# Optimization experiments

Hardware: AMD Instinct MI355X
Metric: run time of the kernel (lower is better)

Reference implementation:

```python
import jax, jax.numpy as jnp
import numpy as np

IMG = 224          # image_size
FMAP = (56, 56)    # feature_map_dims (AdaptiveAvgPool2d((56,56)))
K_REWEIGHT = 3     # self.n_reweight
BLUR_RADIUS = 4    # KNNGaussianBlur(4): kernel 9, sigma 4


def _cdist(a, b):
    # Euclidean pairwise distance, [Na, D] x [Nb, D] -> [Na, Nb]
    a2 = jnp.sum(a * a, axis=1, keepdims=True)            # [Na,1]
    b2 = jnp.sum(b * b, axis=1, keepdims=True).T          # [1,Nb]
    d2 = a2 + b2 - 2.0 * (a @ b.T)
    return jnp.sqrt(jnp.maximum(d2, 0.0))


def _gaussian_blur(x):
    # x: [1,1,H,W]; torchvision GaussianBlur(kernel=9, sigma=4), reflect pad
    r, sigma = BLUR_RADIUS, float(BLUR_RADIUS)
    t = jnp.arange(2 * r + 1, dtype=x.dtype) - r
    g = jnp.exp(-(t * t) / (2.0 * sigma * sigma))
    g = g / jnp.sum(g)
    k2d = jnp.outer(g, g)[None, None]                     # [1,1,9,9]
    xp = jnp.pad(x, ((0, 0), (0, 0), (r, r), (r, r)), mode='reflect')
    return jax.lax.conv_general_dilated(
        xp, k2d, window_strides=(1, 1), padding='VALID',
        dimension_numbers=('NCHW', 'OIHW', 'NCHW'))


def setup_inputs() -> dict:
    key = jax.random.key(0)
    k1, k2 = jax.random.split(key)
    patch = jax.random.normal(k1, (FMAP[0] * FMAP[1], 768), dtype=jnp.float32)
    patch_lib = jax.random.normal(k2, (16384, 768), dtype=jnp.float32)
    mean = jnp.zeros((), dtype=jnp.float32)
    std = jnp.ones((), dtype=jnp.float32)
    return {"patch": patch, "patch_lib": patch_lib, "mean": mean, "std": std}


def reference(patch, patch_lib, mean, std):
    # normalization (method_name != 'Point_MAE' branch)
    p = (patch - mean) / std                               # [N, D]

    dist = _cdist(p, patch_lib)                            # [N, Nlib]
    min_val = jnp.min(dist, axis=1)                        # [N]
    min_idx = jnp.argmin(dist, axis=1)                     # [N]
    s_idx = jnp.argmax(min_val)
    s_star = jnp.max(min_val)

    m_test = p[s_idx]                                      # [D]
    m_star = patch_lib[min_idx[s_idx]]                     # [D]

    # distances of m_star to whole bank, k smallest
    w_dist = jnp.sqrt(jnp.maximum(
        jnp.sum((patch_lib - m_star) ** 2, axis=1), 0.0))  # [Nlib]
    _, nn_idx = jax.lax.top_k(-w_dist, K_REWEIGHT)         # smallest k
    m_star_knn = jnp.linalg.norm(
        m_test[None, :] - patch_lib[nn_idx[1:]], axis=1)   # [k-1]

    D_sqrt = jnp.sqrt(jnp.asarray(patch.shape[1], dtype=p.dtype))
    w = 1.0 - jnp.exp(s_star / D_sqrt) / jnp.sum(jnp.exp(m_star_knn / D_sqrt))
    s = w * s_star

    s_map = min_val.reshape(1, 1, *FMAP)
    s_map = jax.image.resize(s_map, (1, 1, IMG, IMG), method='bilinear')
    s_map = _gaussian_blur(s_map)
    return s, s_map
```

## Files before the change

kernel.cpp:

```cpp
#include <hip/hip_runtime.h>
#include <hip/hip_bf16.h>
#include <stdint.h>

#define N_PATCH 3136
#define N_PATCH_PAD 3328
#define N_LIB   16384
#define DIM     768
#define IMGSZ   224
#define FM      56

#define TILE 256
#define BK 32
#define KT 24
#define MT 13
#define NTILES 64

#define TAILB 64
#define D2_MARGIN 8.0f

typedef __bf16 bf16_t;
typedef __bf16 bf16x8 __attribute__((ext_vector_type(8)));
typedef __bf16 bf16x4_v __attribute__((ext_vector_type(4)));
typedef float  f32x4  __attribute__((ext_vector_type(4)));

#define FLT_MAX_ 3.402823466e+38f

struct Scal {
  unsigned long long approx_max_pack;
  unsigned long long cand_pack[64];
  int cand[64];
  int cand_count;
  int bar[4];
};

__device__ __forceinline__ float wave_reduce_sum(float v) {
#pragma unroll
  for (int s = 32; s > 0; s >>= 1) v += __shfl_xor(v, s, 64);
  return v;
}

__device__ __forceinline__ float wave_reduce_min(float v) {
#pragma unroll
  for (int s = 32; s > 0; s >>= 1) v = fminf(v, __shfl_xor(v, s, 64));
  return v;
}

__device__ __forceinline__ unsigned long long shfl_xor_u64(unsigned long long v, int mask) {
  unsigned lo = (unsigned)v, hi = (unsigned)(v >> 32);
  lo = __shfl_xor(lo, mask, 64);
  hi = __shfl_xor(hi, mask, 64);
  return ((unsigned long long)hi << 32) | lo;
}

__device__ __forceinline__ void async16(const bf16_t* g, bf16_t* l) {
  __builtin_amdgcn_global_load_lds(
      (const __attribute__((address_space(1))) unsigned int*)g,
      (__attribute__((address_space(3))) unsigned int*)l, 16, 0, 0);
}

__device__ __forceinline__ void grid_bar(int* ctr, int nb) {
  __syncthreads();
  if (threadIdx.x == 0) {
    __threadfence();
    atomicAdd(ctr, 1);
    while (atomicAdd(ctr, 0) < nb) __builtin_amdgcn_s_sleep(8);
    __threadfence();
  }
  __syncthreads();
}

__device__ __forceinline__ float bf16u_to_f(unsigned short u) {
  return __uint_as_float(((unsigned)u) << 16);
}

__global__ void prep_kernel(const float* __restrict__ patch, const float* __restrict__ lib,
                            const float* __restrict__ meanp, const float* __restrict__ stdp,
                            bf16_t* __restrict__ pb, bf16_t* __restrict__ lb,
                            float* __restrict__ a2, float* __restrict__ b2, Scal* sc) {
  int t = threadIdx.x;
  int lane = t & 63;
  if (blockIdx.x == 0) {
    if (t < 64) sc->cand_pack[t] = ~0ULL;
    if (t == 64) { sc->approx_max_pack = 0ULL; sc->cand_count = 0; }
    if (t >= 65 && t < 69) sc->bar[t - 65] = 0;
  }
  if (blockIdx.x < N_PATCH / 4) {
    int row = blockIdx.x * 4 + (t >> 6);
    float mu = meanp[0], sd = stdp[0];
    float acc = 0.f;
#pragma unroll
    for (int k = 0; k < 3; k++) {
      float4 v = ((const float4*)(patch + (size_t)row * DIM))[lane + 64 * k];
      v.x = (v.x - mu) / sd; v.y = (v.y - mu) / sd;
      v.z = (v.z - mu) / sd; v.w = (v.w - mu) / sd;
      bf16x4_v o = {(__bf16)v.x, (__bf16)v.y, (__bf16)v.z, (__bf16)v.w};
      *(bf16x4_v*)(pb + (size_t)row * DIM + (lane + 64 * k) * 4) = o;
      acc += v.x*v.x + v.y*v.y + v.z*v.z + v.w*v.w;
    }
    acc = wave_reduce_sum(acc);
    if (lane == 0) a2[row] = acc;
  } else {
    int row = (blockIdx.x - N_PATCH / 4) * 4 + (t >> 6);
    float acc = 0.f;
#pragma unroll
    for (int k = 0; k < 3; k++) {
      float4 v = ((const float4*)(lib + (size_t)row * DIM))[lane + 64 * k];
      bf16x4_v o = {(__bf16)v.x, (__bf16)v.y, (__bf16)v.z, (__bf16)v.w};
      *(bf16x4_v*)(lb + (size_t)row * DIM + (lane + 64 * k) * 4) = o;
      acc += v.x*v.x + v.y*v.y + v.z*v.z + v.w*v.w;
    }
    acc = wave_reduce_sum(acc);
    if (lane == 0) b2[row] = acc;
  }
}

__global__ __launch_bounds__(512, 2)
void gemm_min_kernel(const bf16_t* __restrict__ pb, const bf16_t* __restrict__ lb,
                     const float* __restrict__ a2, const float* __restrict__ b2,
                     float* __restrict__ part) {
  __shared__ __align__(16) bf16_t As[4][TILE * BK];
  __shared__ __align__(16) bf16_t Bs[4][TILE * BK];

  const int t = threadIdx.x;
  const int wave = t >> 6;
  const int lane = t & 63;
  const int l15 = lane & 15;
  const int quad = lane >> 4;
  const int wm = (wave >> 2) * 128;
  const int wn = (wave & 3) * 64;

  const int lid = blockIdx.x;
  const int xcd = lid & 7;
  const int slot = lid >> 3;
  const int ntile = xcd + 8 * (slot / MT);
  const int mtile = slot % MT;
  const int m0 = mtile * TILE;
  const int n0 = ntile * TILE;

  int rA0, kA0, rA1, kA1;
  {
    int c = t, L = c >> 3, s = c & 7, g = s ^ (L & 7);
    rA0 = 2 * L + (g >> 2); kA0 = g & 3;
    c = t + 512; L = c >> 3; s = c & 7; g = s ^ (L & 7);
    rA1 = 2 * L + (g >> 2); kA1 = g & 3;
  }
  int raA0 = m0 + rA0;        if (raA0 > N_PATCH - 1) raA0 = N_PATCH - 1;
  int raA1 = m0 + rA1;        if (raA1 > N_PATCH - 1) raA1 = N_PATCH - 1;
  const bf16_t* gA0 = pb + (size_t)raA0 * DIM + kA0 * 8;
  const bf16_t* gA1 = pb + (size_t)raA1 * DIM + kA1 * 8;
  const bf16_t* gB0 = lb + (size_t)(n0 + rA0) * DIM + kA0 * 8;
  const bf16_t* gB1 = lb + (size_t)(n0 + rA1) * DIM + kA1 * 8;

  auto stage = [&](int kt, int s) {
    const size_t ko = (size_t)kt * BK;
    async16(gA0 + ko, &As[s][0] + (size_t)t * 8);
    async16(gA1 + ko, &As[s][0] + 4096 + (size_t)t * 8);
    async16(gB0 + ko, &Bs[s][0] + (size_t)t * 8);
    async16(gB1 + ko, &Bs[s][0] + 4096 + (size_t)t * 8);
  };

  const int off_lane = (l15 >> 1) * 128 + (((((l15 & 1) << 2) | quad) ^ (l15 >> 1)) << 4);

  f32x4 acc[8][4];
#pragma unroll
  for (int mi = 0; mi < 8; mi++)
#pragma unroll
    for (int ni = 0; ni < 4; ni++) { f32x4 z = {0.f,0.f,0.f,0.f}; acc[mi][ni] = z; }

  stage(0, 0); stage(1, 1); stage(2, 2);

  auto compute = [&](int s) {
    const char* Ab = (const char*)(&As[s][0]);
    const char* Bb = (const char*)(&Bs[s][0]);
    bf16x8 afr[8], bfr[4];
#pragma unroll
    for (int ni = 0; ni < 4; ni++)
      bfr[ni] = *(const bf16x8*)(Bb + (wn + ni * 16) * 64 + off_lane);
#pragma unroll
    for (int mi = 0; mi < 8; mi++)
      afr[mi] = *(const bf16x8*)(Ab + (wm + mi * 16) * 64 + off_lane);
    __builtin_amdgcn_s_setprio(1);
#pragma unroll
    for (int mi = 0; mi < 8; mi++)
#pragma unroll
      for (int ni = 0; ni < 4; ni++)
        acc[mi][ni] = __builtin_amdgcn_mfma_f32_16x16x32_bf16(afr[mi], bfr[ni],
                                                              acc[mi][ni], 0, 0, 0);
    __builtin_amdgcn_s_setprio(0);
  };

  for (int k = 0; k < KT - 3; ++k) {
    asm volatile("s_waitcnt vmcnt(8)" ::: "memory");
    __builtin_amdgcn_s_barrier();
    asm volatile("" ::: "memory");
    stage(k + 3, (k + 3) & 3);
    compute(k & 3);
  }
  asm volatile("s_waitcnt vmcnt(8)" ::: "memory");
  __builtin_amdgcn_s_barrier();
  asm volatile("" ::: "memory");
  compute((KT - 3) & 3);

  asm volatile("s_waitcnt vmcnt(4)" ::: "memory");
  __builtin_amdgcn_s_barrier();
  asm volatile("" ::: "memory");
  compute((KT - 2) & 3);

  asm volatile("s_waitcnt vmcnt(0)" ::: "memory");
  __builtin_amdgcn_s_barrier();
  asm volatile("" ::: "memory");
  compute((KT - 1) & 3);

  __syncthreads();
  unsigned* smin = (unsigned*)&As[0][0];
  if (t < 256) smin[t] = 0xffffffffu;
  __syncthreads();

  float b2n[4];
#pragma unroll
  for (int ni = 0; ni < 4; ni++) b2n[ni] = b2[n0 + wn + ni * 16 + l15];

#pragma unroll
  for (int mi = 0; mi < 8; mi++) {
#pragma unroll
    for (int r = 0; r < 4; r++) {
      int rloc = wm + mi * 16 + quad * 4 + r;
      int mrow = m0 + rloc;
      float a2v = a2[mrow < N_PATCH ? mrow : (N_PATCH - 1)];
      float best = a2v + b2n[0] - 2.0f * acc[mi][0][r];
#pragma unroll
      for (int ni = 1; ni < 4; ni++)
        best = fminf(best, a2v + b2n[ni] - 2.0f * acc[mi][ni][r]);
      best = fmaxf(best, 0.0f);
#pragma unroll
      for (int s = 1; s < 16; s <<= 1)
        best = fminf(best, __shfl_xor(best, s, 64));
      if (l15 == 0) atomicMin(&smin[rloc], __float_as_uint(best));
    }
  }
  __syncthreads();
  if (t < 256) part[(size_t)ntile * N_PATCH_PAD + m0 + t] = __uint_as_float(smin[t]);
}

__device__ __forceinline__ void wave_pick(const Scal* sc, int cnt, int lane,
                                          int* srow, float* sstar, int* ms) {
  unsigned long long pk = 0ULL;
  int rowv = 0, msv = 0;
  if (lane < cnt) {
    unsigned long long cp = sc->cand_pack[lane];
    rowv = sc->cand[lane];
    msv = (int)(cp & 0xffffffffu);
    pk = (cp & 0xffffffff00000000ULL) | (unsigned)(0xffffffffu - (unsigned)rowv);
  }
  unsigned long long m = pk;
#pragma unroll
  for (int s = 1; s < 64; s <<= 1) {
    unsigned long long o = shfl_xor_u64(m, s);
    if (o > m) m = o;
  }
  unsigned long long mask = __ballot(pk == m && lane < cnt);
  int wl = (int)(__ffsll((long long)mask) - 1);
  *srow = __shfl(rowv, wl, 64);
  *ms   = __shfl(msv, wl, 64);
  *sstar = sqrtf(__uint_as_float((unsigned)(m >> 32)));
}

__global__ __launch_bounds__(256, 2)
void tail_kernel(const float* __restrict__ part, float* __restrict__ min_val,
                 const float* __restrict__ patch, const float* __restrict__ lib,
                 const bf16_t* __restrict__ lb,
                 const float* __restrict__ meanp, const float* __restrict__ stdp,
                 Scal* __restrict__ sc, float* __restrict__ wdist2,
                 float* __restrict__ out0, float* __restrict__ outmap) {
  __shared__ union {
    unsigned long long sl[768];
    float rs[40 * 40];
  } sm;
  __shared__ float redbuf[4];
  __shared__ int s_cnt;

  const int t = threadIdx.x;
  const int b = blockIdx.x;
  const int wave = t >> 6, lane = t & 63;

  {
    int row = b * 256 + t;
    if (row < N_PATCH) {
      float m = FLT_MAX_;
#pragma unroll 8
      for (int nt = 0; nt < NTILES; nt++)
        m = fminf(m, part[(size_t)nt * N_PATCH_PAD + row]);
      float v = sqrtf(m);
      min_val[row] = v;
      unsigned long long mp = (((unsigned long long)__float_as_uint(v)) << 32) |
                              (unsigned)(0xffffffffu - (unsigned)row);
      atomicMax(&sc->approx_max_pack, mp);
    }
  }
  grid_bar(&sc->bar[0], TAILB);

  if (b == 0) {
    float amax = __uint_as_float((unsigned)(atomicMax(&sc->approx_max_pack, 0ULL) >> 32));
    for (int i = t; i < N_PATCH; i += 256) {
      if (min_val[i] >= amax - 0.05f) {
        int p = atomicAdd(&sc->cand_count, 1);
        if (p < 64) sc->cand[p] = i;
      }
    }
  }
  grid_bar(&sc->bar[1], TAILB);

  if (t == 0) s_cnt = atomicAdd(&sc->cand_count, 0);
  __syncthreads();
  int cnt = s_cnt; if (cnt > 64) cnt = 64;

  {
    float mu = meanp[0], sd = stdp[0];
    for (int c = 0; c < cnt; c++) {
      int row = sc->cand[c];
      float pv_ = (t < NTILES) ? part[(size_t)t * N_PATCH_PAD + row] : FLT_MAX_;
      pv_ = wave_reduce_min(pv_);
      if (lane == 0) redbuf[wave] = pv_;
      __syncthreads();
      float bmin = fminf(fminf(redbuf[0], redbuf[1]), fminf(redbuf[2], redbuf[3]));
      __syncthreads();

      float4 pv[3];
#pragma unroll
      for (int k = 0; k < 3; k++) {
        float4 v = ((const float4*)(patch + (size_t)row * DIM))[lane + 64 * k];
        v.x = (v.x - mu) / sd; v.y = (v.y - mu) / sd;
        v.z = (v.z - mu) / sd; v.w = (v.w - mu) / sd;
        pv[k] = v;
      }
      int nt = b;
      float pmin = part[(size_t)nt * N_PATCH_PAD + row];
      if (pmin <= bmin + D2_MARGIN) {
        unsigned long long best = ~0ULL;
        int jb = nt * 256 + wave * 64;
        for (int rr = 0; rr < 64; rr++) {
          int j = jb + rr;
          const float4* pl = (const float4*)(lib + (size_t)j * DIM);
          float acc = 0.f;
#pragma unroll
          for (int k = 0; k < 3; k++) {
            float4 l = pl[lane + 64 * k];
            float dx = pv[k].x - l.x, dy = pv[k].y - l.y;
            float dz = pv[k].z - l.z, dw = pv[k].w - l.w;
            acc += dx*dx + dy*dy + dz*dz + dw*dw;
          }
          acc = wave_reduce_sum(acc);
          unsigned long long pk = (((unsigned long long)__float_as_uint(acc)) << 32) | (unsigned)j;
          if (pk < best) best = pk;
        }
        if (lane == 0) atomicMin(&sc->cand_pack[c], best);
      }
    }
  }
  grid_bar(&sc->bar[2], TAILB);

  {
    int srow_, ms; float ss_;
    wave_pick(sc, cnt, lane, &srow_, &ss_, &ms);
    float pm[12];
    const ushort4* pms = (const ushort4*)(lb + (size_t)ms * DIM);
#pragma unroll
    for (int k = 0; k < 3; k++) {
      ushort4 u = pms[lane + 64 * k];
      pm[k*4+0] = bf16u_to_f(u.x); pm[k*4+1] = bf16u_to_f(u.y);
      pm[k*4+2] = bf16u_to_f(u.z); pm[k*4+3] = bf16u_to_f(u.w);
    }
    int jbase = b * 256 + wave * 64;
    for (int rr = 0; rr < 64; rr += 2) {
      int j0 = jbase + rr, j1 = j0 + 1;
      const ushort4* r0 = (const ushort4*)(lb + (size_t)j0 * DIM);
      const ushort4* r1 = (const ushort4*)(lb + (size_t)j1 * DIM);
      float a0 = 0.f, a1 = 0.f;
#pragma unroll
      for (int k = 0; k < 3; k++) {
        ushort4 u0 = r0[lane + 64 * k];
        ushort4 u1 = r1[lane + 64 * k];
        float d;
        d = bf16u_to_f(u0.x) - pm[k*4+0]; a0 += d * d;
        d = bf16u_to_f(u0.y) - pm[k*4+1]; a0 += d * d;
        d = bf16u_to_f(u0.z) - pm[k*4+2]; a0 += d * d;
        d = bf16u_to_f(u0.w) - pm[k*4+3]; a0 += d * d;
        d = bf16u_to_f(u1.x) - pm[k*4+0]; a1 += d * d;
        d = bf16u_to_f(u1.y) - pm[k*4+1]; a1 += d * d;
        d = bf16u_to_f(u1.z) - pm[k*4+2]; a1 += d * d;
        d = bf16u_to_f(u1.w) - pm[k*4+3]; a1 += d * d;
      }
      a0 = wave_reduce_sum(a0);
      a1 = wave_reduce_sum(a1);
      if (lane == 0) { wdist2[j0] = a0; wdist2[j1] = a1; }
    }
  }
  grid_bar(&sc->bar[3], TAILB);

  if (b == 0) {
    unsigned long long b0 = ~0ULL, b1 = ~0ULL, b2 = ~0ULL;
    for (int j = t; j < N_LIB; j += 256) {
      unsigned long long pk = (((unsigned long long)__float_as_uint(wdist2[j])) << 32) | (unsigned)j;
      if (pk < b0)      { b2 = b1; b1 = b0; b0 = pk; }
      else if (pk < b1) { b2 = b1; b1 = pk; }
      else if (pk < b2) { b2 = pk; }
    }
    sm.sl[t * 3 + 0] = b0; sm.sl[t * 3 + 1] = b1; sm.sl[t * 3 + 2] = b2;
    __syncthreads();
    if (t >= 64) return;

    unsigned long long c0 = ~0ULL, c1 = ~0ULL, c2 = ~0ULL;
#pragma unroll
    for (int e = 0; e < 12; e++) {
      unsigned long long pk = sm.sl[t * 12 + e];
      if (pk < c0)      { c2 = c1; c1 = c0; c0 = pk; }
      else if (pk < c1) { c2 = c1; c1 = pk; }
      else if (pk < c2) { c2 = pk; }
    }
    unsigned long long res1 = 0, res2 = 0;
#pragma unroll
    for (int r = 0; r < 3; r++) {
      unsigned long long m = c0;
#pragma unroll
      for (int s = 1; s < 64; s <<= 1) {
        unsigned long long o = shfl_xor_u64(m, s);
        if (o < m) m = o;
      }
      if (r == 1) res1 = m;
      if (r == 2) res2 = m;
      if (c0 == m) { c0 = c1; c1 = c2; c2 = ~0ULL; }
    }
    int nA = (int)(res1 & 0xffffffffu);
    int nB = (int)(res2 & 0xffffffffu);

    int srow, ms2; float sstar;
    wave_pick(sc, cnt, t, &srow, &sstar, &ms2);

    float mu = meanp[0], sd = stdp[0];
    float accA = 0.f, accB = 0.f;
#pragma unroll
    for (int k = 0; k < 3; k++) {
      float4 p4 = ((const float4*)(patch + (size_t)srow * DIM))[t + 64 * k];
      float4 a4 = ((const float4*)(lib + (size_t)nA * DIM))[t + 64 * k];
      float4 b4 = ((const float4*)(lib + (size_t)nB * DIM))[t + 64 * k];
      float px = (p4.x - mu) / sd, py = (p4.y - mu) / sd;
      float pz = (p4.z - mu) / sd, pw = (p4.w - mu) / sd;
      float dax = px - a4.x, day = py - a4.y, daz = pz - a4.z, daw = pw - a4.w;
      float dbx = px - b4.x, dby = py - b4.y, dbz = pz - b4.z, dbw = pw - b4.w;
      accA += dax*dax + day*day + daz*daz + daw*daw;
      accB += dbx*dbx + dby*dby + dbz*dbz + dbw*dbw;
    }
    accA = wave_reduce_sum(accA);
    accB = wave_reduce_sum(accB);
    if (t == 0) {
      float dsq = sqrtf((float)DIM);
      float d1 = sqrtf(accA), d2v = sqrtf(accB);
      float w = 1.0f - expf(sstar / dsq) / (expf(d1 / dsq) + expf(d2v / dsq));
      out0[0] = w * sstar;
    }
    return;
  }

  if (b > 49) return;
  {
    int tile = b - 1;
    int bx = tile % 7, by = tile / 7;
    int ox0 = bx * 32, oy0 = by * 32;

    for (int i = t; i < 1600; i += 256) {
      int ly = i / 40, lx = i % 40;
      int gy = oy0 - 4 + ly; gy = gy < 0 ? 0 : (gy > 223 ? 223 : gy);
      int gx = ox0 - 4 + lx; gx = gx < 0 ? 0 : (gx > 223 ? 223 : gx);
      float sy = fminf(fmaxf(0.25f * gy - 0.375f, 0.0f), 55.0f);
      float sx = fminf(fmaxf(0.25f * gx - 0.375f, 0.0f), 55.0f);
      int y0 = (int)sy; if (y0 > 54) y0 = 54;
      int x0 = (int)sx; if (x0 > 54) x0 = 54;
      float fy = sy - y0, fx = sx - x0;
      float v00 = min_val[y0*FM + x0],     v01 = min_val[y0*FM + x0 + 1];
      float v10 = min_val[(y0+1)*FM + x0], v11 = min_val[(y0+1)*FM + x0 + 1];
      float a = v00 + fx * (v01 - v00);
      float bb = v10 + fx * (v11 - v10);
      sm.rs[i] = a + fy * (bb - a);
    }
    __syncthreads();

    float g[9]; float gs = 0.f;
#pragma unroll
    for (int i = 0; i < 9; i++) { float tt = (float)(i - 4); g[i] = expf(-(tt*tt)/32.0f); gs += g[i]; }
#pragma unroll
    for (int i = 0; i < 9; i++) g[i] /= gs;

    for (int p = t; p < 1024; p += 256) {
      int y = oy0 + p / 32, x = ox0 + (p & 31);
      float acc = 0.f;
#pragma unroll
      for (int dy = 0; dy < 9; dy++) {
        int yy = y + dy - 4;
        yy = yy < 0 ? -yy : (yy > IMGSZ - 1 ? 2*(IMGSZ-1) - yy : yy);
        int lyy = yy - (oy0 - 4);
        float ra = 0.f;
#pragma unroll
        for (int dx = 0; dx < 9; dx++) {
          int xx = x + dx - 4;
          xx = xx < 0 ? -xx : (xx > IMGSZ - 1 ? 2*(IMGSZ-1) - xx : xx);
          ra += g[dx] * sm.rs[lyy * 40 + (xx - (ox0 - 4))];
        }
        acc += g[dy] * ra;
      }
      outmap[y * IMGSZ + x] = acc;
    }
  }
}

extern "C" void kernel_launch(void* const* d_in, const int* in_sizes, int n_in,
                              void* d_out, int out_size, void* d_ws, size_t ws_size,
                              hipStream_t stream) {
  const float* patch = (const float*)d_in[0];
  const float* lib   = (const float*)d_in[1];
  const float* meanp = (const float*)d_in[2];
  const float* stdp  = (const float*)d_in[3];
  float* out = (float*)d_out;

  char* ws = (char*)d_ws;
  size_t off = 0;
  auto alloc = [&](size_t bytes) -> void* {
    void* p = ws + off;
    off = (off + bytes + 255) & ~(size_t)255;
    return p;
  };
  bf16_t* pb      = (bf16_t*)alloc((size_t)N_PATCH * DIM * sizeof(bf16_t));
  bf16_t* lb      = (bf16_t*)alloc((size_t)N_LIB * DIM * sizeof(bf16_t));
  float* a2       = (float*)alloc(N_PATCH * sizeof(float));
  float* b2       = (float*)alloc(N_LIB * sizeof(float));
  float* part     = (float*)alloc((size_t)N_PATCH_PAD * NTILES * sizeof(float));
  float* min_val  = (float*)alloc(N_PATCH * sizeof(float));
  float* wdist2   = (float*)alloc(N_LIB * sizeof(float));
  Scal*  sc       = (Scal*)alloc(sizeof(Scal));

  prep_kernel<<<N_PATCH / 4 + N_LIB / 4, 256, 0, stream>>>(patch, lib, meanp, stdp,
                                                           pb, lb, a2, b2, sc);
  gemm_min_kernel<<<MT * NTILES, 512, 0, stream>>>(pb, lb, a2, b2, part);
  tail_kernel<<<TAILB, 256, 0, stream>>>(part, min_val, patch, lib, lb, meanp, stdp,
                                         sc, wdist2, out, out + 1);
}
```

Before: 336.5 us.

## Make GEMM-min kernel persistent with atomic work queue and split-phase k-steps

Launches a fixed grid of 256 persistent blocks that pull tile indices from an atomic counter instead of one block per tile. Each k-step is split into two halves, with A and B global loads for the future stage spread across them and separated by barriers, so that MFMA work overlaps more with memory traffic. This is meant to reduce tail-wave imbalance and exposed load latency. It adds per-tile atomics and extra barriers, and it drops the previous XCD-aware tile ordering, which may hurt L2 reuse.

Measured after the change: 340.0 us. Within noise of the previous version (+1.0%).

```diff
diff --git a/kernel.cpp b/kernel.cpp
--- a/kernel.cpp
+++ b/kernel.cpp
@@ -14,6 +14,8 @@
 #define KT 24
 #define MT 13
 #define NTILES 64
+#define NWORK (MT * NTILES)
+#define GEMMB 256
 
 #define TAILB 64
 #define D2_MARGIN 8.0f
@@ -31,6 +33,7 @@
   int cand[64];
   int cand_count;
   int bar[4];
+  int work;
 };
 
 __device__ __forceinline__ float wave_reduce_sum(float v) {
@@ -83,6 +86,7 @@
     if (t < 64) sc->cand_pack[t] = ~0ULL;
     if (t == 64) { sc->approx_max_pack = 0ULL; sc->cand_count = 0; }
     if (t >= 65 && t < 69) sc->bar[t - 65] = 0;
+    if (t == 69) sc->work = 0;
   }
   if (blockIdx.x < N_PATCH / 4) {
     int row = blockIdx.x * 4 + (t >> 6);
@@ -117,9 +121,10 @@
 __global__ __launch_bounds__(512, 2)
 void gemm_min_kernel(const bf16_t* __restrict__ pb, const bf16_t* __restrict__ lb,
                      const float* __restrict__ a2, const float* __restrict__ b2,
-                     float* __restrict__ part) {
+                     float* __restrict__ part, Scal* __restrict__ sc) {
   __shared__ __align__(16) bf16_t As[4][TILE * BK];
   __shared__ __align__(16) bf16_t Bs[4][TILE * BK];
+  __shared__ int sw;
 
   const int t = threadIdx.x;
   const int wave = t >> 6;
@@ -129,14 +134,6 @@
   const int wm = (wave >> 2) * 128;
   const int wn = (wave & 3) * 64;
 
-  const int lid = blockIdx.x;
-  const int xcd = lid & 7;
-  const int slot = lid >> 3;
-  const int ntile = xcd + 8 * (slot / MT);
-  const int mtile = slot % MT;
-  const int m0 = mtile * TILE;
-  const int n0 = ntile * TILE;
-
   int rA0, kA0, rA1, kA1;
   {
     int c = t, L = c >> 3, s = c & 7, g = s ^ (L & 7);
@@ -144,102 +141,142 @@
     c = t + 512; L = c >> 3; s = c & 7; g = s ^ (L & 7);
     rA1 = 2 * L + (g >> 2); kA1 = g & 3;
   }
-  int raA0 = m0 + rA0;        if (raA0 > N_PATCH - 1) raA0 = N_PATCH - 1;
-  int raA1 = m0 + rA1;        if (raA1 > N_PATCH - 1) raA1 = N_PATCH - 1;
-  const bf16_t* gA0 = pb + (size_t)raA0 * DIM + kA0 * 8;
-  const bf16_t* gA1 = pb + (size_t)raA1 * DIM + kA1 * 8;
-  const bf16_t* gB0 = lb + (size_t)(n0 + rA0) * DIM + kA0 * 8;
-  const bf16_t* gB1 = lb + (size_t)(n0 + rA1) * DIM + kA1 * 8;
-
-  auto stage = [&](int kt, int s) {
-    const size_t ko = (size_t)kt * BK;
-    async16(gA0 + ko, &As[s][0] + (size_t)t * 8);
-    async16(gA1 + ko, &As[s][0] + 4096 + (size_t)t * 8);
-    async16(gB0 + ko, &Bs[s][0] + (size_t)t * 8);
-    async16(gB1 + ko, &Bs[s][0] + 4096 + (size_t)t * 8);
-  };
 
   const int off_lane = (l15 >> 1) * 128 + (((((l15 & 1) << 2) | quad) ^ (l15 >> 1)) << 4);
 
-  f32x4 acc[8][4];
-#pragma unroll
-  for (int mi = 0; mi < 8; mi++)
-#pragma unroll
-    for (int ni = 0; ni < 4; ni++) { f32x4 z = {0.f,0.f,0.f,0.f}; acc[mi][ni] = z; }
-
-  stage(0, 0); stage(1, 1); stage(2, 2);
-
-  auto compute = [&](int s) {
-    const char* Ab = (const char*)(&As[s][0]);
-    const char* Bb = (const char*)(&Bs[s][0]);
-    bf16x8 afr[8], bfr[4];
-#pragma unroll
-    for (int ni = 0; ni < 4; ni++)
-      bfr[ni] = *(const bf16x8*)(Bb + (wn + ni * 16) * 64 + off_lane);
+  for (;;) {
+    if (t == 0) sw = atomicAdd(&sc->work, 1);
+    __syncthreads();
+    const int w = sw;
+    if (w >= NWORK) break;
+
+    const int ntile = w / MT;
+    const int mtile = w - ntile * MT;
+    const int m0 = mtile * TILE;
+    const int n0 = ntile * TILE;
+
+    int raA0 = m0 + rA0;        if (raA0 > N_PATCH - 1) raA0 = N_PATCH - 1;
+    int raA1 = m0 + rA1;        if (raA1 > N_PATCH - 1) raA1 = N_PATCH - 1;
+    const bf16_t* gA0 = pb + (size_t)raA0 * DIM + kA0 * 8;
+    const bf16_t* gA1 = pb + (size_t)raA1 * DIM + kA1 * 8;
+    const bf16_t* gB0 = lb + (size_t)(n0 + rA0) * DIM + kA0 * 8;
+    const bf16_t* gB1 = lb + (size_t)(n0 + rA1) * DIM + kA1 * 8;
+
+    f32x4 acc[8][4];
 #pragma unroll
     for (int mi = 0; mi < 8; mi++)
-      afr[mi] = *(const bf16x8*)(Ab + (wm + mi * 16) * 64 + off_lane);
-    __builtin_amdgcn_s_setprio(1);
-#pragma unroll
-    for (int mi = 0; mi < 8; mi++)
+#pragma unroll
+      for (int ni = 0; ni < 4; ni++) { f32x4 z = {0.f,0.f,0.f,0.f}; acc[mi][ni] = z; }
+
+#pragma unroll
+    for (int p = 0; p < 3; p++) {
+      const size_t ko = (size_t)p * BK;
+      async16(gA0 + ko, &As[p][0] + (size_t)t * 8);
+      async16(gA1 + ko, &As[p][0] + 4096 + (size_t)t * 8);
+      async16(gB0 + ko, &Bs[p][0] + (size_t)t * 8);
+      async16(gB1 + ko, &Bs[p][0] + 4096 + (size_t)t * 8);
+    }
+
+    auto kstep = [&](int s, int kst) {
+      const char* Ab = (const char*)(&As[s][0]);
+      const char* Bb = (const char*)(&Bs[s][0]);
+      bf16x8 bfr[4], afr[4];
 #pragma unroll
       for (int ni = 0; ni < 4; ni++)
-        acc[mi][ni] = __builtin_amdgcn_mfma_f32_16x16x32_bf16(afr[mi], bfr[ni],
-                                                              acc[mi][ni], 0, 0, 0);
-    __builtin_amdgcn_s_setprio(0);
-  };
-
-  for (int k = 0; k < KT - 3; ++k) {
+        bfr[ni] = *(const bf16x8*)(Bb + (wn + ni * 16) * 64 + off_lane);
+#pragma unroll
+      for (int mi = 0; mi < 4; mi++)
+        afr[mi] = *(const bf16x8*)(Ab + (wm + mi * 16) * 64 + off_lane);
+      if (kst >= 0) {
+        const size_t ko = (size_t)kst * BK;
+        bf16_t* dst = &As[kst & 3][0];
+        async16(gA0 + ko, dst + (size_t)t * 8);
+        async16(gA1 + ko, dst + 4096 + (size_t)t * 8);
+      }
+      asm volatile("" ::: "memory");
+      __builtin_amdgcn_s_barrier();
+      __builtin_amdgcn_s_setprio(1);
+#pragma unroll
+      for (int mi = 0; mi < 4; mi++)
+#pragma unroll
+        for (int ni = 0; ni < 4; ni++)
+          acc[mi][ni] = __builtin_amdgcn_mfma_f32_16x16x32_bf16(afr[mi], bfr[ni],
+                                                                acc[mi][ni], 0, 0, 0);
+      __builtin_amdgcn_s_setprio(0);
+      __builtin_amdgcn_s_barrier();
+      bf16x8 afr2[4];
+#pragma unroll
+      for (int mi = 0; mi < 4; mi++)
+        afr2[mi] = *(const bf16x8*)(Ab + (wm + 64 + mi * 16) * 64 + off_lane);
+      if (kst >= 0) {
+        const size_t ko = (size_t)kst * BK;
+        bf16_t* dst = &Bs[kst & 3][0];
+        async16(gB0 + ko, dst + (size_t)t * 8);
+        async16(gB1 + ko, dst + 4096 + (size_t)t * 8);
+      }
+      asm volatile("" ::: "memory");
+      __builtin_amdgcn_s_barrier();
+      __builtin_amdgcn_s_setprio(1);
+#pragma unroll
+      for (int mi = 0; mi < 4; mi++)
+#pragma unroll
+        for (int ni = 0; ni < 4; ni++)
+          acc[4 + mi][ni] = __builtin_amdgcn_mfma_f32_16x16x32_bf16(afr2[mi], bfr[ni],
+                                                                    acc[4 + mi][ni], 0, 0, 0);
+      __builtin_amdgcn_s_setprio(0);
+    };
+
+    for (int k = 0; k < KT - 3; ++k) {
+      asm volatile("s_waitcnt vmcnt(8)" ::: "memory");
+      __builtin_amdgcn_s_barrier();
+      asm volatile("" ::: "memory");
+      kstep(k & 3, k + 3);
+    }
     asm volatile("s_waitcnt vmcnt(8)" ::: "memory");
     __builtin_amdgcn_s_barrier();
     asm volatile("" ::: "memory");
-    stage(k + 3, (k + 3) & 3);
-    compute(k & 3);
-  }
-  asm volatile("s_waitcnt vmcnt(8)" ::: "memory");
-  __builtin_amdgcn_s_barrier();
-  asm volatile("" ::: "memory");
-  compute((KT - 3) & 3);
-
-  asm volatile("s_waitcnt vmcnt(4)" ::: "memory");
-  __builtin_amdgcn_s_barrier();
-  asm volatile("" ::: "memory");
-  compute((KT - 2) & 3);
-
-  asm volatile("s_waitcnt vmcnt(0)" ::: "memory");
-  __builtin_amdgcn_s_barrier();
-  asm volatile("" ::: "memory");
-  compute((KT - 1) & 3);
-
-  __syncthreads();
-  unsigned* smin = (unsigned*)&As[0][0];
-  if (t < 256) smin[t] = 0xffffffffu;
-  __syncthreads();
-
-  float b2n[4];
-#pragma unroll
-  for (int ni = 0; ni < 4; ni++) b2n[ni] = b2[n0 + wn + ni * 16 + l15];
-
-#pragma unroll
-  for (int mi = 0; mi < 8; mi++) {
-#pragma unroll
-    for (int r = 0; r < 4; r++) {
-      int rloc = wm + mi * 16 + quad * 4 + r;
-      int mrow = m0 + rloc;
-      float a2v = a2[mrow < N_PATCH ? mrow : (N_PATCH - 1)];
-      float best = a2v + b2n[0] - 2.0f * acc[mi][0][r];
-#pragma unroll
-      for (int ni = 1; ni < 4; ni++)
-        best = fminf(best, a2v + b2n[ni] - 2.0f * acc[mi][ni][r]);
-      best = fmaxf(best, 0.0f);
-#pragma unroll
-      for (int s = 1; s < 16; s <<= 1)
-        best = fminf(best, __shfl_xor(best, s, 64));
-      if (l15 == 0) atomicMin(&smin[rloc], __float_as_uint(best));
-    }
-  }
-  __syncthreads();
-  if (t < 256) part[(size_t)ntile * N_PATCH_PAD + m0 + t] = __uint_as_float(smin[t]);
+    kstep((KT - 3) & 3, -1);
+
+    asm volatile("s_waitcnt vmcnt(4)" ::: "memory");
+    __builtin_amdgcn_s_barrier();
+    asm volatile("" ::: "memory");
+    kstep((KT - 2) & 3, -1);
+
+    asm volatile("s_waitcnt vmcnt(0)" ::: "memory");
+    __builtin_amdgcn_s_barrier();
+    asm volatile("" ::: "memory");
+    kstep((KT - 1) & 3, -1);
+
+    __syncthreads();
+    unsigned* smin = (unsigned*)&As[0][0];
+    if (t < 256) smin[t] = 0xffffffffu;
+    __syncthreads();
+
+    float b2n[4];
+#pragma unroll
+    for (int ni = 0; ni < 4; ni++) b2n[ni] = b2[n0 + wn + ni * 16 + l15];
+
+#pragma unroll
+    for (int mi = 0; mi < 8; mi++) {
+#pragma unroll
+      for (int r = 0; r < 4; r++) {
+        int rloc = wm + mi * 16 + quad * 4 + r;
+        int mrow = m0 + rloc;
+        float a2v = a2[mrow < N_PATCH ? mrow : (N_PATCH - 1)];
+        float best = a2v + b2n[0] - 2.0f * acc[mi][0][r];
+#pragma unroll
+        for (int ni = 1; ni < 4; ni++)
+          best = fminf(best, a2v + b2n[ni] - 2.0f * acc[mi][ni][r]);
+        best = fmaxf(best, 0.0f);
+#pragma unroll
+        for (int s = 1; s < 16; s <<= 1)
+          best = fminf(best, __shfl_xor(best, s, 64));
+        if (l15 == 0) atomicMin(&smin[rloc], __float_as_uint(best));
+      }
+    }
+    __syncthreads();
+    if (t < 256) part[(size_t)ntile * N_PATCH_PAD + m0 + t] = __uint_as_float(smin[t]);
+  }
 }
 
 __device__ __forceinline__ void wave_pick(const Scal* sc, int cnt, int lane,
@@ -539,7 +576,7 @@
 
   prep_kernel<<<N_PATCH / 4 + N_LIB / 4, 256, 0, stream>>>(patch, lib, meanp, stdp,
                                                            pb, lb, a2, b2, sc);
-  gemm_min_kernel<<<MT * NTILES, 512, 0, stream>>>(pb, lb, a2, b2, part);
+  gemm_min_kernel<<<GEMMB, 512, 0, stream>>>(pb, lb, a2, b2, part, sc);
   tail_kernel<<<TAILB, 256, 0, stream>>>(part, min_val, patch, lib, lb, meanp, stdp,
                                          sc, wdist2, out, out + 1);
 }
```
